# Performance work log

Measured on AMD Instinct MI355X. Metric: run time of the kernel, lower is better.

The kernel has to match this reference:

```python
import jax, jax.numpy as jnp
import numpy as np

H = 2048        # hidden_size
HS = 4096       # shared_expert_intermediate_size
P = 1024        # private_expert_intermediate_size
E = 8           # num_experts
TOP_K = 2       # num_experts_per_tok
B, S = 4, 2048


def setup_inputs() -> dict:
    key = jax.random.key(0)
    ks = jax.random.split(key, 8)
    sc = 0.02
    return {
        "hidden_states": jax.random.normal(ks[0], (B, S, H), jnp.float32),
        "router_w": jax.random.normal(ks[1], (E, H), jnp.float32) * sc,
        "sg_w": jax.random.normal(ks[2], (HS, H), jnp.float32) * sc,   # shared_gate_proj
        "sd_w": jax.random.normal(ks[3], (H, HS), jnp.float32) * sc,   # shared_down_proj
        "pg_w": jax.random.normal(ks[4], (E, H), jnp.float32) * sc,    # private_expert_gate per expert
        "g_w": jax.random.normal(ks[5], (E, P, H), jnp.float32) * sc,  # expert gate_proj
        "d_w": jax.random.normal(ks[6], (E, H, P), jnp.float32) * sc,  # expert down_proj
    }


def reference(hidden_states, router_w, sg_w, sd_w, pg_w, g_w, d_w):
    b, s, h = hidden_states.shape
    x = hidden_states.reshape(-1, h)                       # [T, H]
    T = x.shape[0]

    router_logits = x @ router_w.T                         # [T, E]
    routing_probs = jax.nn.softmax(router_logits.astype(jnp.float32), axis=-1)
    routing_weights, selected = jax.lax.top_k(routing_probs, TOP_K)  # [T, K]
    routing_weights = routing_weights.astype(x.dtype)

    # token -> expert combine weights (scatter of top-k weights), [T, E]
    combine = jnp.zeros((T, E), x.dtype).at[jnp.arange(T)[:, None], selected].add(routing_weights)

    # shared expert path: identical for every expert, compute once per token
    h1 = jnp.maximum(x @ sg_w.T, 0.0) @ sd_w.T             # [T, H]

    # per-expert private gate: sigmoid(Linear(H->1)) per expert, stacked -> [T, E]
    g = jax.nn.sigmoid(h1 @ pg_w.T)

    # expert gate_proj applied to (g * h1); linearity: (g*h1) @ Wg == g * (h1 @ Wg)
    a = jnp.einsum('th,eph->tep', h1, g_w)                 # [T, E, P]
    act = jnp.maximum(g[:, :, None] * a, 0.0)              # relu

    # down_proj, weighted combine over experts: [T, H]
    out = jnp.einsum('tep,ehp,te->th', act, d_w, combine)
    final = out.reshape(b, s, h)

    # aux load-balancing loss
    eps = 1e-9
    importance = routing_probs.sum(axis=0)                 # [E]
    load = jnp.zeros((E,), jnp.float32).at[selected.reshape(-1)].add(1.0)
    imp = importance / (importance.sum() + eps)
    ld = load / (load.sum() + eps)
    aux_loss = E * jnp.sum(imp * ld)

    return final, router_logits, aux_loss
```

## Files before the change

kernel.cpp:

```cpp
#include <hip/hip_runtime.h>

typedef _Float16 f16x8 __attribute__((ext_vector_type(8)));
typedef float f32x4 __attribute__((ext_vector_type(4)));
typedef unsigned short u16x8 __attribute__((ext_vector_type(8)));

constexpr int T = 8192, H = 2048, HS = 4096, P = 1024, E = 8;

constexpr size_t LOGITS_OFF = (size_t)T * H;
constexpr size_t AUX_OFF    = LOGITS_OFF + (size_t)T * E;

constexpr size_t OFF_SGW  = 0;
constexpr size_t OFF_SDW  = OFF_SGW  + (size_t)HS * H * 2;
constexpr size_t OFF_GW   = OFF_SDW  + (size_t)H * HS * 2;
constexpr size_t OFF_DW   = OFF_GW   + (size_t)E * P * H * 2;
constexpr size_t OFF_BIG0 = OFF_DW   + (size_t)E * H * P * 2;
constexpr size_t OFF_BIG1 = OFF_BIG0 + (size_t)T * H * 2;
constexpr size_t OFF_H1   = OFF_BIG1 + (size_t)T * HS * 2;
constexpr size_t OFF_GALL = OFF_H1   + (size_t)T * H * 2;
constexpr size_t OFF_CNT  = OFF_GALL + (size_t)T * E * 4;
constexpr size_t OFF_IMP  = OFF_CNT  + 256;
constexpr size_t OFF_OFFS = OFF_IMP  + 256;
constexpr size_t OFF_SEL  = OFF_OFFS + 256;
constexpr size_t OFF_SELW = OFF_SEL  + (size_t)T * 2 * 4;
constexpr size_t OFF_POS  = OFF_SELW + (size_t)T * 2 * 4;
constexpr size_t OFF_AID  = OFF_POS  + (size_t)T * 2 * 4;
constexpr size_t OFF_TOK  = OFF_AID  + (size_t)T * 2 * 4;
constexpr size_t OFF_WOF  = OFF_TOK  + (size_t)T * 2 * 4;

__device__ __forceinline__ unsigned short f2h(float f) {
  return __builtin_bit_cast(unsigned short, (_Float16)f);
}
__device__ __forceinline__ float h2f(unsigned short u) {
  return (float)__builtin_bit_cast(_Float16, u);
}
__device__ __forceinline__ void gload16(const void* g, void* l) {
  __builtin_amdgcn_global_load_lds((__attribute__((address_space(1))) void*)g,
                                   (__attribute__((address_space(3))) void*)l, 16, 0, 0);
}

__global__ void cvt4_kernel(const float* __restrict__ s0, const float* __restrict__ s1,
                            const float* __restrict__ s2, const float* __restrict__ s3,
                            unsigned short* __restrict__ d,
                            int* __restrict__ counts, float* __restrict__ imp) {
  if (blockIdx.x == 0 && threadIdx.x < E) { counts[threadIdx.x] = 0; imp[threadIdx.x] = 0.f; }
  const int i = blockIdx.x * 256 + threadIdx.x;
  constexpr int N0 = (HS * H) / 4;
  constexpr int N1 = N0 + (H * HS) / 4;
  constexpr int N2 = N1 + (E * P * H) / 4;
  float4 v;
  if (i < N0)      v = ((const float4*)s0)[i];
  else if (i < N1) v = ((const float4*)s1)[i - N0];
  else if (i < N2) v = ((const float4*)s2)[i - N1];
  else             v = ((const float4*)s3)[i - N2];
  ushort4 o;
  o.x = f2h(v.x); o.y = f2h(v.y); o.z = f2h(v.z); o.w = f2h(v.w);
  ((ushort4*)d)[i] = o;
}

__global__ void router_kernel(const float* __restrict__ x, const float* __restrict__ rw,
                              float* __restrict__ logits, int* __restrict__ counts,
                              float* __restrict__ impg, int* __restrict__ sel,
                              float* __restrict__ selw, int* __restrict__ posA,
                              unsigned short* __restrict__ x16) {
  __shared__ float sRW[E * H];
  __shared__ float sImp[E];
  __shared__ int sCnt[E], sBase[E];
  __shared__ int sE[16][2], sS[16][2];
  const int tid = threadIdx.x, lane = tid & 63, wid = tid >> 6;
  if (tid < E) { sImp[tid] = 0.f; sCnt[tid] = 0; }
#pragma unroll
  for (int i = 0; i < (E * H / 4) / 256; ++i)
    ((float4*)sRW)[i * 256 + tid] = ((const float4*)rw)[i * 256 + tid];
  __syncthreads();

  for (int i = 0; i < 4; ++i) {
    const int ti = wid * 4 + i;
    const int t = blockIdx.x * 16 + ti;
    float p[E];
#pragma unroll
    for (int e = 0; e < E; ++e) p[e] = 0.f;
    const float4* xr = (const float4*)(x + (size_t)t * H);
#pragma unroll
    for (int q = 0; q < 8; ++q) {
      float4 xv = xr[q * 64 + lane];
      ushort4 xo;
      xo.x = f2h(xv.x); xo.y = f2h(xv.y); xo.z = f2h(xv.z); xo.w = f2h(xv.w);
      ((ushort4*)(x16 + (size_t)t * H))[q * 64 + lane] = xo;
#pragma unroll
      for (int e = 0; e < E; ++e) {
        float4 wv = ((const float4*)sRW)[e * 512 + q * 64 + lane];
        p[e] += xv.x * wv.x + xv.y * wv.y + xv.z * wv.z + xv.w * wv.w;
      }
    }
#pragma unroll
    for (int e = 0; e < E; ++e)
#pragma unroll
      for (int o = 32; o; o >>= 1) p[e] += __shfl_xor(p[e], o);

    if (lane == 0) {
      float mx = p[0];
#pragma unroll
      for (int e = 1; e < E; ++e) mx = fmaxf(mx, p[e]);
      float pe[E], s = 0.f;
#pragma unroll
      for (int e = 0; e < E; ++e) { pe[e] = expf(p[e] - mx); s += pe[e]; }
      float inv = 1.f / s;
      int i1 = 0; float b1 = pe[0];
#pragma unroll
      for (int e = 1; e < E; ++e) if (pe[e] > b1) { b1 = pe[e]; i1 = e; }
      int i2 = -1; float b2 = -1.f;
#pragma unroll
      for (int e = 0; e < E; ++e) if (e != i1 && pe[e] > b2) { b2 = pe[e]; i2 = e; }
#pragma unroll
      for (int e = 0; e < E; ++e) logits[(size_t)t * E + e] = p[e];
#pragma unroll
      for (int e = 0; e < E; ++e) atomicAdd(&sImp[e], pe[e] * inv);
      int s1 = atomicAdd(&sCnt[i1], 1);
      int s2 = atomicAdd(&sCnt[i2], 1);
      sel[t * 2] = i1; sel[t * 2 + 1] = i2;
      selw[t * 2] = b1 * inv; selw[t * 2 + 1] = b2 * inv;
      sE[ti][0] = i1; sE[ti][1] = i2; sS[ti][0] = s1; sS[ti][1] = s2;
    }
  }
  __syncthreads();
  if (tid < E) {
    sBase[tid] = atomicAdd(&counts[tid], sCnt[tid]);
    atomicAdd(&impg[tid], sImp[tid]);
  }
  __syncthreads();
  if (lane == 0) {
    for (int i = 0; i < 4; ++i) {
      int ti = wid * 4 + i, t = blockIdx.x * 16 + ti;
      posA[t * 2]     = sBase[sE[ti][0]] + sS[ti][0];
      posA[t * 2 + 1] = sBase[sE[ti][1]] + sS[ti][1];
    }
  }
}

__global__ void fill_kernel(const int* __restrict__ sel, const float* __restrict__ selw,
                            const int* __restrict__ posA, const int* __restrict__ counts,
                            const float* __restrict__ imp,
                            int* __restrict__ offs, float* __restrict__ aux_out,
                            int* __restrict__ tok_of, float* __restrict__ w_of,
                            int* __restrict__ aid_of) {
  int c[E];
#pragma unroll
  for (int e = 0; e < E; ++e) c[e] = counts[e];
  int pre[E + 1];
  pre[0] = 0;
#pragma unroll
  for (int e = 0; e < E; ++e) pre[e + 1] = pre[e] + c[e];

  const int idx = blockIdx.x * 256 + threadIdx.x;
  if (blockIdx.x == 0 && threadIdx.x == 0) {
#pragma unroll
    for (int e = 0; e <= E; ++e) offs[e] = pre[e];
    float simp = 0.f, sld = (float)pre[E];
#pragma unroll
    for (int e = 0; e < E; ++e) simp += imp[e];
    float aux = 0.f;
#pragma unroll
    for (int e = 0; e < E; ++e)
      aux += (imp[e] / (simp + 1e-9f)) * ((float)c[e] / (sld + 1e-9f));
    aux_out[0] = (float)E * aux;
  }
  if (idx >= T * 2) return;
  int t = idx >> 1;
  int e = sel[idx];
  int aid = pre[e] + posA[idx];
  tok_of[aid] = t;
  w_of[aid] = selw[idx];
  aid_of[idx] = aid;
}

__global__ void g_kernel(const unsigned short* __restrict__ h1, const float* __restrict__ pgw,
                         float* __restrict__ g_all) {
  const int lane = threadIdx.x & 63, wid = threadIdx.x >> 6;
  const int t = blockIdx.x * 4 + wid;
  float p[E];
#pragma unroll
  for (int e = 0; e < E; ++e) p[e] = 0.f;
#pragma unroll
  for (int i = 0; i < 4; ++i) {
    const int h = (i * 64 + lane) * 8;
    u16x8 hv = *(const u16x8*)(h1 + (size_t)t * H + h);
    float hf[8];
#pragma unroll
    for (int j = 0; j < 8; ++j) hf[j] = h2f(hv[j]);
#pragma unroll
    for (int e = 0; e < E; ++e) {
      const float4* wp = (const float4*)(pgw + (size_t)e * H + h);
      float4 w0 = wp[0], w1 = wp[1];
      p[e] += hf[0] * w0.x + hf[1] * w0.y + hf[2] * w0.z + hf[3] * w0.w +
              hf[4] * w1.x + hf[5] * w1.y + hf[6] * w1.z + hf[7] * w1.w;
    }
  }
#pragma unroll
  for (int e = 0; e < E; ++e)
#pragma unroll
    for (int o = 32; o; o >>= 1) p[e] += __shfl_xor(p[e], o);
  if (lane == 0) {
#pragma unroll
    for (int e = 0; e < E; ++e) g_all[(size_t)t * E + e] = 1.f / (1.f + expf(-p[e]));
  }
}

template <int MODE>
__global__ __launch_bounds__(256, 3) void gemm_bt(
    const unsigned short* __restrict__ A, const unsigned short* __restrict__ B,
    unsigned short* __restrict__ Cout, const int* __restrict__ tok_of,
    const float* __restrict__ g_all, const float* __restrict__ w_of,
    const int* __restrict__ offs, int N, int K) {
  __shared__ alignas(128) char sA[128 * 64 * 2];
  __shared__ alignas(128) char sB[128 * 64 * 2];
  const int tid = threadIdx.x, lane = tid & 63, wid = tid >> 6;
  const int wr = wid >> 1, wc = wid & 1;

  int bm = blockIdx.x, bn = blockIdx.y;
  int rowStart = 0, cnt = 1 << 30, e = 0;
  const unsigned short* Bp = B;
  if (MODE <= 1) {
    if (gridDim.x == 64) {
      const int wg = blockIdx.y * 64 + blockIdx.x;
      const int xcd = wg & 7;
      const int idx = wg >> 3;
      bm = xcd * 8 + (idx & 7);
      bn = idx >> 3;
    }
  } else {
    e = blockIdx.z;
    rowStart = offs[e];
    cnt = offs[e + 1] - rowStart;
    if (bm * 128 >= cnt) return;
    Bp = B + (size_t)e * N * K;
  }

  const char* aSrc[4];
  const char* bSrc[4];
  char* dA[4];
  char* dB[4];
#pragma unroll
  for (int it = 0; it < 4; ++it) {
    const int ci = wid * 4 + it;
    const int o = ci * 1024 + lane * 16;
    const int row = o >> 7;
    const int cbs = (o & 127) ^ ((row & 7) << 4);
    dA[it] = sA + ci * 1024;
    dB[it] = sB + ci * 1024;
    long arow;
    if (MODE <= 1) {
      arow = (long)(bm * 128 + row);
    } else if (MODE == 2) {
      int grow = bm * 128 + row;
      arow = (grow < cnt) ? (long)tok_of[rowStart + grow] : 0L;
    } else {
      int grow = bm * 128 + row;
      arow = (grow < cnt) ? (long)(rowStart + grow) : (long)rowStart;
    }
    aSrc[it] = (const char*)A + arow * (long)K * 2 + cbs;
    bSrc[it] = (const char*)Bp + (long)(bn * 128 + row) * (long)K * 2 + cbs;
  }

  f32x4 acc[4][4];
#pragma unroll
  for (int a_ = 0; a_ < 4; ++a_)
#pragma unroll
    for (int b_ = 0; b_ < 4; ++b_) acc[a_][b_] = (f32x4){0.f, 0.f, 0.f, 0.f};

  for (int k0 = 0; k0 < K; k0 += 64) {
#pragma unroll
    for (int it = 0; it < 4; ++it) {
      gload16(aSrc[it] + (size_t)k0 * 2, dA[it]);
      gload16(bSrc[it] + (size_t)k0 * 2, dB[it]);
    }
    __syncthreads();
#pragma unroll
    for (int kk = 0; kk < 2; ++kk) {
      f16x8 af[4], bfr[4];
      const int c0 = kk * 64 + (lane >> 4) * 16;
#pragma unroll
      for (int mt = 0; mt < 4; ++mt) {
        const int r = wr * 64 + mt * 16 + (lane & 15);
        af[mt] = *(const f16x8*)(sA + r * 128 + (c0 ^ ((r & 7) << 4)));
      }
#pragma unroll
      for (int nt = 0; nt < 4; ++nt) {
        const int r = wc * 64 + nt * 16 + (lane & 15);
        bfr[nt] = *(const f16x8*)(sB + r * 128 + (c0 ^ ((r & 7) << 4)));
      }
#pragma unroll
      for (int mt = 0; mt < 4; ++mt)
#pragma unroll
        for (int nt = 0; nt < 4; ++nt)
          acc[mt][nt] = __builtin_amdgcn_mfma_f32_16x16x32_f16(af[mt], bfr[nt], acc[mt][nt], 0, 0, 0);
    }
    __syncthreads();
  }

  const int colBase = bn * 128 + wc * 64 + (lane & 15);
#pragma unroll
  for (int mt = 0; mt < 4; ++mt) {
#pragma unroll
    for (int j = 0; j < 4; ++j) {
      const int rloc = wr * 64 + mt * 16 + (lane >> 4) * 4 + j;
      const int grow = bm * 128 + rloc;
      if (MODE <= 1) {
        const size_t base = (size_t)grow * N;
#pragma unroll
        for (int nt = 0; nt < 4; ++nt) {
          float v = acc[mt][nt][j];
          if (MODE == 0) v = fmaxf(v, 0.f);
          Cout[base + colBase + nt * 16] = f2h(v);
        }
      } else if (MODE == 2) {
        if (grow < cnt) {
          const int aid = rowStart + grow;
          const float g = g_all[(size_t)tok_of[aid] * E + e];
          const size_t base = (size_t)aid * N;
#pragma unroll
          for (int nt = 0; nt < 4; ++nt) {
            float v = fmaxf(g * acc[mt][nt][j], 0.f);
            Cout[base + colBase + nt * 16] = f2h(v);
          }
        }
      } else {
        if (grow < cnt) {
          const int aid = rowStart + grow;
          const float w = w_of[aid];
          const size_t base = (size_t)aid * N;
#pragma unroll
          for (int nt = 0; nt < 4; ++nt)
            Cout[base + colBase + nt * 16] = f2h(w * acc[mt][nt][j]);
        }
      }
    }
  }
}

__global__ void combine_kernel(const unsigned short* __restrict__ slot,
                               const int* __restrict__ aid_of, float* __restrict__ out) {
  const int idx = blockIdx.x * 256 + threadIdx.x;
  const int t = idx >> 8;
  const int c8 = (idx & 255) * 8;
  const int a0 = aid_of[t * 2], a1 = aid_of[t * 2 + 1];
  u16x8 v0 = *(const u16x8*)(slot + (size_t)a0 * H + c8);
  u16x8 v1 = *(const u16x8*)(slot + (size_t)a1 * H + c8);
  float4 f0, f1;
  f0.x = h2f(v0[0]) + h2f(v1[0]); f0.y = h2f(v0[1]) + h2f(v1[1]);
  f0.z = h2f(v0[2]) + h2f(v1[2]); f0.w = h2f(v0[3]) + h2f(v1[3]);
  f1.x = h2f(v0[4]) + h2f(v1[4]); f1.y = h2f(v0[5]) + h2f(v1[5]);
  f1.z = h2f(v0[6]) + h2f(v1[6]); f1.w = h2f(v0[7]) + h2f(v1[7]);
  float4* op = (float4*)(out + (size_t)t * H + c8);
  op[0] = f0; op[1] = f1;
}

extern "C" void kernel_launch(void* const* d_in, const int* in_sizes, int n_in,
                              void* d_out, int out_size, void* d_ws, size_t ws_size,
                              hipStream_t stream) {
  const float* x   = (const float*)d_in[0];
  const float* rw  = (const float*)d_in[1];
  const float* sgw = (const float*)d_in[2];
  const float* sdw = (const float*)d_in[3];
  const float* pgw = (const float*)d_in[4];
  const float* gw  = (const float*)d_in[5];
  const float* dw  = (const float*)d_in[6];
  float* out = (float*)d_out;
  char* wsb = (char*)d_ws;

  unsigned short* sgw16 = (unsigned short*)(wsb + OFF_SGW);
  unsigned short* sdw16 = (unsigned short*)(wsb + OFF_SDW);
  unsigned short* gw16  = (unsigned short*)(wsb + OFF_GW);
  unsigned short* dw16  = (unsigned short*)(wsb + OFF_DW);
  unsigned short* x16   = (unsigned short*)(wsb + OFF_BIG0);
  unsigned short* act   = (unsigned short*)(wsb + OFF_BIG0);
  unsigned short* c1    = (unsigned short*)(wsb + OFF_BIG1);
  unsigned short* slot  = (unsigned short*)(wsb + OFF_BIG1);
  unsigned short* h1    = (unsigned short*)(wsb + OFF_H1);
  float* gall  = (float*)(wsb + OFF_GALL);
  int*   cnts  = (int*)(wsb + OFF_CNT);
  float* imp   = (float*)(wsb + OFF_IMP);
  int*   offs  = (int*)(wsb + OFF_OFFS);
  int*   sel   = (int*)(wsb + OFF_SEL);
  float* selw  = (float*)(wsb + OFF_SELW);
  int*   posA  = (int*)(wsb + OFF_POS);
  int*   aidof = (int*)(wsb + OFF_AID);
  int*   tokof = (int*)(wsb + OFF_TOK);
  float* wof   = (float*)(wsb + OFF_WOF);

  cvt4_kernel<<<(HS * H + H * HS + E * P * H + E * H * P) / 4 / 256, 256, 0, stream>>>(
      sgw, sdw, gw, dw, sgw16, cnts, imp);

  router_kernel<<<T / 16, 256, 0, stream>>>(x, rw, out + LOGITS_OFF, cnts, imp, sel, selw, posA, x16);

  fill_kernel<<<(T * 2) / 256, 256, 0, stream>>>(sel, selw, posA, cnts, imp, offs, out + AUX_OFF,
                                                 tokof, wof, aidof);

  gemm_bt<0><<<dim3(T / 128, HS / 128), 256, 0, stream>>>(x16, sgw16, c1, nullptr, nullptr, nullptr, nullptr, HS, H);
  gemm_bt<1><<<dim3(T / 128, H / 128), 256, 0, stream>>>(c1, sdw16, h1, nullptr, nullptr, nullptr, nullptr, H, HS);
  g_kernel<<<T / 4, 256, 0, stream>>>(h1, pgw, gall);
  gemm_bt<2><<<dim3(T / 128, P / 128, E), 256, 0, stream>>>(h1, gw16, act, tokof, gall, nullptr, offs, P, H);
  gemm_bt<3><<<dim3(T / 128, H / 128, E), 256, 0, stream>>>(act, dw16, slot, tokof, nullptr, wof, offs, H, P);

  combine_kernel<<<(T * 256) / 256, 256, 0, stream>>>(slot, aidof, out);
}
```

Before: 736.0 us.

## Replace atomic expert slot assignment with deterministic per-block scan; raise gemm occupancy

The router kernel no longer takes global atomics to claim expert slots. Each block now writes per-expert counts and in-block ranks, and a new single-block scan kernel computes per-block bases, expert offsets and the aux loss. This gives a deterministic token ordering and removes contended global atomics, at the cost of one extra small kernel launch. Separately, the gemm launch bound goes from 3 to 4 blocks per CU, which may force register spills.

```diff
diff --git a/kernel.cpp b/kernel.cpp
--- a/kernel.cpp
+++ b/kernel.cpp
@@ -5,6 +5,7 @@
 typedef unsigned short u16x8 __attribute__((ext_vector_type(8)));
 
 constexpr int T = 8192, H = 2048, HS = 4096, P = 1024, E = 8;
+constexpr int RBLK = 512;
 
 constexpr size_t LOGITS_OFF = (size_t)T * H;
 constexpr size_t AUX_OFF    = LOGITS_OFF + (size_t)T * E;
@@ -17,8 +18,7 @@
 constexpr size_t OFF_BIG1 = OFF_BIG0 + (size_t)T * H * 2;
 constexpr size_t OFF_H1   = OFF_BIG1 + (size_t)T * HS * 2;
 constexpr size_t OFF_GALL = OFF_H1   + (size_t)T * H * 2;
-constexpr size_t OFF_CNT  = OFF_GALL + (size_t)T * E * 4;
-constexpr size_t OFF_IMP  = OFF_CNT  + 256;
+constexpr size_t OFF_IMP  = OFF_GALL + (size_t)T * E * 4;
 constexpr size_t OFF_OFFS = OFF_IMP  + 256;
 constexpr size_t OFF_SEL  = OFF_OFFS + 256;
 constexpr size_t OFF_SELW = OFF_SEL  + (size_t)T * 2 * 4;
@@ -26,6 +26,8 @@
 constexpr size_t OFF_AID  = OFF_POS  + (size_t)T * 2 * 4;
 constexpr size_t OFF_TOK  = OFF_AID  + (size_t)T * 2 * 4;
 constexpr size_t OFF_WOF  = OFF_TOK  + (size_t)T * 2 * 4;
+constexpr size_t OFF_BCNT = OFF_WOF  + (size_t)T * 2 * 4;
+constexpr size_t OFF_BBAS = OFF_BCNT + (size_t)RBLK * E * 4;
 
 __device__ __forceinline__ unsigned short f2h(float f) {
   return __builtin_bit_cast(unsigned short, (_Float16)f);
@@ -40,9 +42,8 @@
 
 __global__ void cvt4_kernel(const float* __restrict__ s0, const float* __restrict__ s1,
                             const float* __restrict__ s2, const float* __restrict__ s3,
-                            unsigned short* __restrict__ d,
-                            int* __restrict__ counts, float* __restrict__ imp) {
-  if (blockIdx.x == 0 && threadIdx.x < E) { counts[threadIdx.x] = 0; imp[threadIdx.x] = 0.f; }
+                            unsigned short* __restrict__ d, float* __restrict__ imp) {
+  if (blockIdx.x == 0 && threadIdx.x < E) imp[threadIdx.x] = 0.f;
   const int i = blockIdx.x * 256 + threadIdx.x;
   constexpr int N0 = (HS * H) / 4;
   constexpr int N1 = N0 + (H * HS) / 4;
@@ -58,16 +59,17 @@
 }
 
 __global__ void router_kernel(const float* __restrict__ x, const float* __restrict__ rw,
-                              float* __restrict__ logits, int* __restrict__ counts,
-                              float* __restrict__ impg, int* __restrict__ sel,
-                              float* __restrict__ selw, int* __restrict__ posA,
+                              float* __restrict__ logits, float* __restrict__ impg,
+                              int* __restrict__ sel, float* __restrict__ selw,
+                              int* __restrict__ posA, int* __restrict__ block_cnt,
                               unsigned short* __restrict__ x16) {
   __shared__ float sRW[E * H];
   __shared__ float sImp[E];
-  __shared__ int sCnt[E], sBase[E];
-  __shared__ int sE[16][2], sS[16][2];
+  __shared__ int sE[16][2];
+  __shared__ int sRank[16][2];
+  __shared__ int sBC[E];
   const int tid = threadIdx.x, lane = tid & 63, wid = tid >> 6;
-  if (tid < E) { sImp[tid] = 0.f; sCnt[tid] = 0; }
+  if (tid < E) sImp[tid] = 0.f;
 #pragma unroll
   for (int i = 0; i < (E * H / 4) / 256; ++i)
     ((float4*)sRW)[i * 256 + tid] = ((const float4*)rw)[i * 256 + tid];
@@ -115,59 +117,82 @@
       for (int e = 0; e < E; ++e) logits[(size_t)t * E + e] = p[e];
 #pragma unroll
       for (int e = 0; e < E; ++e) atomicAdd(&sImp[e], pe[e] * inv);
-      int s1 = atomicAdd(&sCnt[i1], 1);
-      int s2 = atomicAdd(&sCnt[i2], 1);
       sel[t * 2] = i1; sel[t * 2 + 1] = i2;
       selw[t * 2] = b1 * inv; selw[t * 2 + 1] = b2 * inv;
-      sE[ti][0] = i1; sE[ti][1] = i2; sS[ti][0] = s1; sS[ti][1] = s2;
-    }
+      sE[ti][0] = i1; sE[ti][1] = i2;
+    }
+  }
+  __syncthreads();
+  if (tid == 0) {
+    int bc[E];
+#pragma unroll
+    for (int e = 0; e < E; ++e) bc[e] = 0;
+    for (int ti = 0; ti < 16; ++ti) {
+      sRank[ti][0] = bc[sE[ti][0]]++;
+      sRank[ti][1] = bc[sE[ti][1]]++;
+    }
+#pragma unroll
+    for (int e = 0; e < E; ++e) sBC[e] = bc[e];
   }
   __syncthreads();
   if (tid < E) {
-    sBase[tid] = atomicAdd(&counts[tid], sCnt[tid]);
+    block_cnt[blockIdx.x * E + tid] = sBC[tid];
     atomicAdd(&impg[tid], sImp[tid]);
   }
+  if (tid < 32) {
+    const int ti = tid >> 1, k = tid & 1;
+    posA[(blockIdx.x * 16 + ti) * 2 + k] = sRank[ti][k];
+  }
+}
+
+__global__ void scan_kernel(const int* __restrict__ block_cnt, const float* __restrict__ imp,
+                            int* __restrict__ block_base, int* __restrict__ offs,
+                            float* __restrict__ aux_out) {
+  const int lane = threadIdx.x & 63, w = threadIdx.x >> 6;
+  __shared__ int sTot[E];
+  int carry = 0;
+  for (int c = 0; c < RBLK / 64; ++c) {
+    const int b = c * 64 + lane;
+    const int v = block_cnt[b * E + w];
+    int xv = v;
+#pragma unroll
+    for (int off = 1; off < 64; off <<= 1) {
+      int n = __shfl_up(xv, off);
+      if (lane >= off) xv += n;
+    }
+    block_base[b * E + w] = carry + xv - v;
+    carry += __shfl(xv, 63);
+  }
+  if (lane == 0) sTot[w] = carry;
   __syncthreads();
-  if (lane == 0) {
-    for (int i = 0; i < 4; ++i) {
-      int ti = wid * 4 + i, t = blockIdx.x * 16 + ti;
-      posA[t * 2]     = sBase[sE[ti][0]] + sS[ti][0];
-      posA[t * 2 + 1] = sBase[sE[ti][1]] + sS[ti][1];
-    }
+  if (threadIdx.x == 0) {
+    int pre[E + 1];
+    pre[0] = 0;
+#pragma unroll
+    for (int e = 0; e < E; ++e) pre[e + 1] = pre[e] + sTot[e];
+#pragma unroll
+    for (int e = 0; e <= E; ++e) offs[e] = pre[e];
+    float simp = 0.f, sld = (float)pre[E];
+#pragma unroll
+    for (int e = 0; e < E; ++e) simp += imp[e];
+    float aux = 0.f;
+#pragma unroll
+    for (int e = 0; e < E; ++e)
+      aux += (imp[e] / (simp + 1e-9f)) * ((float)sTot[e] / (sld + 1e-9f));
+    aux_out[0] = (float)E * aux;
   }
 }
 
 __global__ void fill_kernel(const int* __restrict__ sel, const float* __restrict__ selw,
-                            const int* __restrict__ posA, const int* __restrict__ counts,
-                            const float* __restrict__ imp,
-                            int* __restrict__ offs, float* __restrict__ aux_out,
+                            const int* __restrict__ posA, const int* __restrict__ block_base,
+                            const int* __restrict__ offs,
                             int* __restrict__ tok_of, float* __restrict__ w_of,
                             int* __restrict__ aid_of) {
-  int c[E];
-#pragma unroll
-  for (int e = 0; e < E; ++e) c[e] = counts[e];
-  int pre[E + 1];
-  pre[0] = 0;
-#pragma unroll
-  for (int e = 0; e < E; ++e) pre[e + 1] = pre[e] + c[e];
-
   const int idx = blockIdx.x * 256 + threadIdx.x;
-  if (blockIdx.x == 0 && threadIdx.x == 0) {
-#pragma unroll
-    for (int e = 0; e <= E; ++e) offs[e] = pre[e];
-    float simp = 0.f, sld = (float)pre[E];
-#pragma unroll
-    for (int e = 0; e < E; ++e) simp += imp[e];
-    float aux = 0.f;
-#pragma unroll
-    for (int e = 0; e < E; ++e)
-      aux += (imp[e] / (simp + 1e-9f)) * ((float)c[e] / (sld + 1e-9f));
-    aux_out[0] = (float)E * aux;
-  }
   if (idx >= T * 2) return;
-  int t = idx >> 1;
-  int e = sel[idx];
-  int aid = pre[e] + posA[idx];
+  const int t = idx >> 1;
+  const int e = sel[idx];
+  const int aid = offs[e] + block_base[(t >> 4) * E + e] + posA[idx];
   tok_of[aid] = t;
   w_of[aid] = selw[idx];
   aid_of[idx] = aid;
@@ -206,7 +231,7 @@
 }
 
 template <int MODE>
-__global__ __launch_bounds__(256, 3) void gemm_bt(
+__global__ __launch_bounds__(256, 4) void gemm_bt(
     const unsigned short* __restrict__ A, const unsigned short* __restrict__ B,
     unsigned short* __restrict__ Cout, const int* __restrict__ tok_of,
     const float* __restrict__ g_all, const float* __restrict__ w_of,
@@ -377,7 +402,6 @@
   unsigned short* slot  = (unsigned short*)(wsb + OFF_BIG1);
   unsigned short* h1    = (unsigned short*)(wsb + OFF_H1);
   float* gall  = (float*)(wsb + OFF_GALL);
-  int*   cnts  = (int*)(wsb + OFF_CNT);
   float* imp   = (float*)(wsb + OFF_IMP);
   int*   offs  = (int*)(wsb + OFF_OFFS);
   int*   sel   = (int*)(wsb + OFF_SEL);
@@ -386,14 +410,17 @@
   int*   aidof = (int*)(wsb + OFF_AID);
   int*   tokof = (int*)(wsb + OFF_TOK);
   float* wof   = (float*)(wsb + OFF_WOF);
+  int*   bcnt  = (int*)(wsb + OFF_BCNT);
+  int*   bbase = (int*)(wsb + OFF_BBAS);
 
   cvt4_kernel<<<(HS * H + H * HS + E * P * H + E * H * P) / 4 / 256, 256, 0, stream>>>(
-      sgw, sdw, gw, dw, sgw16, cnts, imp);
-
-  router_kernel<<<T / 16, 256, 0, stream>>>(x, rw, out + LOGITS_OFF, cnts, imp, sel, selw, posA, x16);
-
-  fill_kernel<<<(T * 2) / 256, 256, 0, stream>>>(sel, selw, posA, cnts, imp, offs, out + AUX_OFF,
-                                                 tokof, wof, aidof);
+      sgw, sdw, gw, dw, sgw16, imp);
+
+  router_kernel<<<RBLK, 256, 0, stream>>>(x, rw, out + LOGITS_OFF, imp, sel, selw, posA, bcnt, x16);
+
+  scan_kernel<<<1, 512, 0, stream>>>(bcnt, imp, bbase, offs, out + AUX_OFF);
+
+  fill_kernel<<<(T * 2) / 256, 256, 0, stream>>>(sel, selw, posA, bbase, offs, tokof, wof, aidof);
 
   gemm_bt<0><<<dim3(T / 128, HS / 128), 256, 0, stream>>>(x16, sgw16, c1, nullptr, nullptr, nullptr, nullptr, HS, H);
   gemm_bt<1><<<dim3(T / 128, H / 128), 256, 0, stream>>>(c1, sdw16, h1, nullptr, nullptr, nullptr, nullptr, H, HS);
```

Measured after the change: 764.4 us. +3.9%, slower.
